# Optimization experiments

Hardware: AMD Instinct MI355X
Metric: run time of the kernel (lower is better)

## Reference

```python
import jax, jax.numpy as jnp
import numpy as np

# POLLU: 25 reactions, 20 species. Each flux r_i = k_i * C[a_i] * C[b_i],
# where index 20 points at a constant-ones row (unimolecular reactions).
ONES_ROW = 20
IDX_A = np.array([0, 1, 4, 6, 6, 6, 8, 8, 10, 10, 12, 9, 13, 0, 2, 3, 3, 15, 15, 16, 18, 18, 0, 18, 19], dtype=np.int32)
IDX_B = np.array([ONES_ROW, 3, 1, ONES_ROW, ONES_ROW, 5, ONES_ROW, 5, 1, 0, ONES_ROW, 1, ONES_ROW, 5, ONES_ROW, ONES_ROW, ONES_ROW, ONES_ROW, ONES_ROW, 5, ONES_ROW, ONES_ROW, 3, 0, ONES_ROW], dtype=np.int32)

def _stoich():
    # species -> list of (coef, 1-based reaction id), transcribed from dy0..dy19
    ent = {
        0: [(-1,1),(-1,10),(-1,14),(-1,23),(-1,24),(1,2),(1,3),(1,9),(1,11),(1,12),(1,22),(1,25)],
        1: [(-1,2),(-1,3),(-1,9),(-1,12),(1,1),(1,21)],
        2: [(-1,15),(1,1),(1,17),(1,19),(1,22)],
        3: [(-1,2),(-1,16),(-1,17),(-1,23),(1,15)],
        4: [(-1,3),(2,4),(1,6),(1,7),(1,13),(1,20)],
        5: [(-1,6),(-1,8),(-1,14),(-1,20),(1,3),(2,18)],
        6: [(-1,4),(-1,5),(-1,6),(1,13)],
        7: [(1,4),(1,5),(1,6),(1,7)],
        8: [(-1,7),(-1,8)],
        9: [(-1,12),(1,7),(1,9)],
        10: [(-1,9),(-1,10),(1,8),(1,11)],
        11: [(1,9)],
        12: [(-1,11),(1,10)],
        13: [(-1,13),(1,12)],
        14: [(1,14)],
        15: [(-1,18),(-1,19),(1,16)],
        16: [(-1,20)],
        17: [(1,20)],
        18: [(-1,21),(-1,22),(-1,24),(1,23),(1,25)],
        19: [(-1,25),(1,24)],
    }
    S = np.zeros((20, 25), dtype=np.float32)
    for sp, lst in ent.items():
        for c, r in lst:
            S[sp, r - 1] += c
    return S

S = _stoich()  # [20 species, 25 reactions]
B = 2_000_000


def setup_inputs() -> dict:
    key = jax.random.key(0)
    k1, k2 = jax.random.split(key)
    conc_in = jax.random.uniform(k1, (20, B), dtype=jnp.float32)
    k = jax.random.uniform(k2, (25,), dtype=jnp.float32)
    t = jnp.zeros((1,), dtype=jnp.float32)
    return {"t": t, "conc_in": conc_in, "k": k}


def reference(t, conc_in, k):
    # conc_in: [20, B]. Append ones row so every flux is a product of two gathers.
    C = jnp.concatenate([conc_in, jnp.ones((1, conc_in.shape[1]), conc_in.dtype)], axis=0)  # [21, B]
    flux = k[:, None] * C[IDX_A] * C[IDX_B]  # [25, B]
    dy = jnp.einsum('sr,rb->bs', jnp.asarray(S, dtype=conc_in.dtype), flux)  # [B, 20]
    return dy
```

## Files before the change

### kernel.cpp

```cpp
#include <hip/hip_runtime.h>

#define B_TOTAL 2000000
#define RS 260
#define CPB 1024

__global__ __launch_bounds__(256) void pollu_kernel(
    const float* __restrict__ conc,
    const float* __restrict__ k,
    float* __restrict__ out)
{
    __shared__ __align__(16) float lds[20 * RS];

    const int t = threadIdx.x;
    const int base = blockIdx.x * CPB;
    const int ncols = min(CPB, B_TOTAL - base);

    const float k0 = k[0],  k1 = k[1],  k2 = k[2],  k3 = k[3],  k4 = k[4];
    const float k5 = k[5],  k6 = k[6],  k7 = k[7],  k8 = k[8],  k9 = k[9];
    const float k10 = k[10], k11 = k[11], k12 = k[12], k13 = k[13], k14 = k[14];
    const float k15 = k[15], k16 = k[16], k17 = k[17], k18 = k[18], k19 = k[19];
    const float k20 = k[20], k21 = k[21], k22 = k[22], k23 = k[23], k24 = k[24];

#define POLLU_FLUX_DY(C)                                                      \
        const float f1  = k0  * C(0);                                         \
        const float f2  = k1  * C(1)  * C(3);                                 \
        const float f3  = k2  * C(4)  * C(1);                                 \
        const float f4  = k3  * C(6);                                         \
        const float f5  = k4  * C(6);                                         \
        const float f6  = k5  * C(6)  * C(5);                                 \
        const float f7  = k6  * C(8);                                         \
        const float f8  = k7  * C(8)  * C(5);                                 \
        const float f9  = k8  * C(10) * C(1);                                 \
        const float f10 = k9  * C(10) * C(0);                                 \
        const float f11 = k10 * C(12);                                        \
        const float f12 = k11 * C(9)  * C(1);                                 \
        const float f13 = k12 * C(13);                                        \
        const float f14 = k13 * C(0)  * C(5);                                 \
        const float f15 = k14 * C(2);                                         \
        const float f16 = k15 * C(3);                                         \
        const float f17 = k16 * C(3);                                         \
        const float f18 = k17 * C(15);                                        \
        const float f19 = k18 * C(15);                                        \
        const float f20 = k19 * C(16) * C(5);                                 \
        const float f21 = k20 * C(18);                                        \
        const float f22 = k21 * C(18);                                        \
        const float f23 = k22 * C(0)  * C(3);                                 \
        const float f24 = k23 * C(18) * C(0);                                 \
        const float f25 = k24 * C(19);                                        \
        C(0)  = -f1 - f10 - f14 - f23 - f24 + f2 + f3 + f9 + f11 + f12 + f22 + f25; \
        C(1)  = -f2 - f3 - f9 - f12 + f1 + f21;                               \
        C(2)  = -f15 + f1 + f17 + f19 + f22;                                  \
        C(3)  = -f2 - f16 - f17 - f23 + f15;                                  \
        C(4)  = -f3 + 2.0f * f4 + f6 + f7 + f13 + f20;                        \
        C(5)  = -f6 - f8 - f14 - f20 + f3 + 2.0f * f18;                       \
        C(6)  = -f4 - f5 - f6 + f13;                                          \
        C(7)  =  f4 + f5 + f6 + f7;                                           \
        C(8)  = -f7 - f8;                                                     \
        C(9)  = -f12 + f7 + f9;                                               \
        C(10) = -f9 - f10 + f8 + f11;                                         \
        C(11) =  f9;                                                          \
        C(12) = -f11 + f10;                                                   \
        C(13) = -f13 + f12;                                                   \
        C(14) =  f14;                                                         \
        C(15) = -f18 - f19 + f16;                                             \
        C(16) = -f20;                                                         \
        C(17) =  f20;                                                         \
        C(18) = -f21 - f22 - f24 + f23 + f25;                                 \
        C(19) = -f25 + f24;

#define CX(s) c4[s].x
#define CY(s) c4[s].y
#define CZ(s) c4[s].z
#define CW(s) c4[s].w
#define CA(s) c[s]

    if (ncols == CPB) {
        float4 c4[20];
        const size_t off = (size_t)base + (size_t)(4 * t);
#pragma unroll
        for (int s = 0; s < 20; ++s)
            c4[s] = *(const float4*)(conc + (size_t)s * B_TOTAL + off);

        { POLLU_FLUX_DY(CX) }
        { POLLU_FLUX_DY(CY) }
        { POLLU_FLUX_DY(CZ) }
        { POLLU_FLUX_DY(CW) }

        float4* outv = (float4*)out;
        const int wave = t >> 6;
        const int lane = t & 63;
#pragma unroll
        for (int p = 0; p < 4; ++p) {
            __syncthreads();
            if (wave == p) {
#pragma unroll
                for (int s = 0; s < 20; ++s)
                    *(float4*)&lds[s * RS + 4 * lane] = c4[s];
            }
            __syncthreads();
            const int passBase = blockIdx.x * 5120 + p * 1280;
#pragma unroll
            for (int i = 0; i < 5; ++i) {
                const int J = i * 256 + t;
                const int q = J / 5;
                const int r = 4 * (J % 5);
                outv[passBase + J] = make_float4(lds[(r + 0) * RS + q],
                                                 lds[(r + 1) * RS + q],
                                                 lds[(r + 2) * RS + q],
                                                 lds[(r + 3) * RS + q]);
            }
        }
    } else {
        for (int col = base + t; col < B_TOTAL; col += 256) {
            float c[20];
#pragma unroll
            for (int s = 0; s < 20; ++s) c[s] = conc[(size_t)s * B_TOTAL + (size_t)col];
            { POLLU_FLUX_DY(CA) }
#pragma unroll
            for (int s = 0; s < 20; ++s) out[(size_t)col * 20 + s] = c[s];
        }
    }
}

extern "C" void kernel_launch(void* const* d_in, const int* in_sizes, int n_in,
                              void* d_out, int out_size, void* d_ws, size_t ws_size,
                              hipStream_t stream) {
    const float* conc = (const float*)d_in[1];
    const float* k    = (const float*)d_in[2];
    float* out        = (float*)d_out;

    const int block = 256;
    const int grid  = (B_TOTAL + CPB - 1) / CPB;
    pollu_kernel<<<grid, block, 0, stream>>>(conc, k, out);
}
```

Measured before the change: 277.3 us.

## Use persistent blocks with register-prefetched tiles and one column per thread

Replaces the one-shot grid of 1024-column blocks with 512 persistent blocks, each looping over a contiguous range of 256-column tiles. The next tile's 20 species are loaded into registers while the current tile is computed and transposed through LDS. Each thread now handles one column per tile using scalar loads instead of float4 loads, and the LDS layout changes to row-per-column with padding 21. The aim is to hide load latency and cut launch and tail overhead, at the cost of narrower loads and more barriers per column processed.

```diff
diff --git a/kernel.cpp b/kernel.cpp
--- a/kernel.cpp
+++ b/kernel.cpp
@@ -1,19 +1,24 @@
 #include <hip/hip_runtime.h>
 
 #define B_TOTAL 2000000
-#define RS 260
-#define CPB 1024
+#define PAD 21
+#define NBLK 512
+#define NTILES 7813
 
 __global__ __launch_bounds__(256) void pollu_kernel(
     const float* __restrict__ conc,
     const float* __restrict__ k,
     float* __restrict__ out)
 {
-    __shared__ __align__(16) float lds[20 * RS];
+    __shared__ float lds[256 * PAD];
 
     const int t = threadIdx.x;
-    const int base = blockIdx.x * CPB;
-    const int ncols = min(CPB, B_TOTAL - base);
+    const int blk = blockIdx.x;
+
+    const int q = NTILES / NBLK;
+    const int r = NTILES - q * NBLK;
+    const int t0 = blk * q + (blk < r ? blk : r);
+    const int t1 = t0 + q + (blk < r ? 1 : 0);
 
     const float k0 = k[0],  k1 = k[1],  k2 = k[2],  k3 = k[3],  k4 = k[4];
     const float k5 = k[5],  k6 = k[6],  k7 = k[7],  k8 = k[8],  k9 = k[9];
@@ -68,56 +73,60 @@
         C(18) = -f21 - f22 - f24 + f23 + f25;                                 \
         C(19) = -f25 + f24;
 
-#define CX(s) c4[s].x
-#define CY(s) c4[s].y
-#define CZ(s) c4[s].z
-#define CW(s) c4[s].w
-#define CA(s) c[s]
+#define CC(s) cc[s]
 
-    if (ncols == CPB) {
-        float4 c4[20];
-        const size_t off = (size_t)base + (size_t)(4 * t);
+    float cc[20], cn[20];
+
+    {
+        const int col = t0 * 256 + t;
+        if (col < B_TOTAL) {
 #pragma unroll
-        for (int s = 0; s < 20; ++s)
-            c4[s] = *(const float4*)(conc + (size_t)s * B_TOTAL + off);
+            for (int s = 0; s < 20; ++s) cc[s] = conc[(size_t)s * B_TOTAL + (size_t)col];
+        } else {
+#pragma unroll
+            for (int s = 0; s < 20; ++s) cc[s] = 0.0f;
+        }
+    }
 
-        { POLLU_FLUX_DY(CX) }
-        { POLLU_FLUX_DY(CY) }
-        { POLLU_FLUX_DY(CZ) }
-        { POLLU_FLUX_DY(CW) }
+    float4* outv = (float4*)out;
 
-        float4* outv = (float4*)out;
-        const int wave = t >> 6;
-        const int lane = t & 63;
+    for (int tt = t0; tt < t1; ++tt) {
+        const bool hasNext = (tt + 1 < t1);
+        if (hasNext) {
+            const int col = (tt + 1) * 256 + t;
+            if (col < B_TOTAL) {
 #pragma unroll
-        for (int p = 0; p < 4; ++p) {
-            __syncthreads();
-            if (wave == p) {
+                for (int s = 0; s < 20; ++s) cn[s] = conc[(size_t)s * B_TOTAL + (size_t)col];
+            } else {
 #pragma unroll
-                for (int s = 0; s < 20; ++s)
-                    *(float4*)&lds[s * RS + 4 * lane] = c4[s];
-            }
-            __syncthreads();
-            const int passBase = blockIdx.x * 5120 + p * 1280;
-#pragma unroll
-            for (int i = 0; i < 5; ++i) {
-                const int J = i * 256 + t;
-                const int q = J / 5;
-                const int r = 4 * (J % 5);
-                outv[passBase + J] = make_float4(lds[(r + 0) * RS + q],
-                                                 lds[(r + 1) * RS + q],
-                                                 lds[(r + 2) * RS + q],
-                                                 lds[(r + 3) * RS + q]);
+                for (int s = 0; s < 20; ++s) cn[s] = 0.0f;
             }
         }
-    } else {
-        for (int col = base + t; col < B_TOTAL; col += 256) {
-            float c[20];
+
+        { POLLU_FLUX_DY(CC) }
+
+        __syncthreads();
 #pragma unroll
-            for (int s = 0; s < 20; ++s) c[s] = conc[(size_t)s * B_TOTAL + (size_t)col];
-            { POLLU_FLUX_DY(CA) }
+        for (int s = 0; s < 20; ++s) lds[t * PAD + s] = cc[s];
+        __syncthreads();
+
+        const int nvalid = min(256, B_TOTAL - tt * 256);
+        const int nF4 = nvalid * 5;
+        const int baseF4 = tt * 1280;
 #pragma unroll
-            for (int s = 0; s < 20; ++s) out[(size_t)col * 20 + s] = c[s];
+        for (int i = 0; i < 5; ++i) {
+            const int J = i * 256 + t;
+            if (J < nF4) {
+                const int q2 = J / 5;
+                const int r2 = 4 * (J % 5);
+                const float* p = &lds[q2 * PAD + r2];
+                outv[baseF4 + J] = make_float4(p[0], p[1], p[2], p[3]);
+            }
+        }
+
+        if (hasNext) {
+#pragma unroll
+            for (int s = 0; s < 20; ++s) cc[s] = cn[s];
         }
     }
 }
@@ -129,7 +138,5 @@
     const float* k    = (const float*)d_in[2];
     float* out        = (float*)d_out;
 
-    const int block = 256;
-    const int grid  = (B_TOTAL + CPB - 1) / CPB;
-    pollu_kernel<<<grid, block, 0, stream>>>(conc, k, out);
+    pollu_kernel<<<NBLK, 256, 0, stream>>>(conc, k, out);
 }
```

Result: slower. 288.2 us (+4.0%).
